# Kernel optimization log

Measured on AMD Instinct MI355X. Metric: run time of the kernel, lower is better.

Reference implementation:

```python
import jax, jax.numpy as jnp
import numpy as np
from jax import lax

BN_EPS = 1e-5


def conv(x, w, b, pad):
    # x: NCHW, w: OIHW
    y = lax.conv_general_dilated(x, w, (1, 1), [(pad, pad), (pad, pad)],
                                 dimension_numbers=('NCHW', 'OIHW', 'NCHW'))
    return y + b[None, :, None, None]


def conv_t(x, w, b):
    # ConvTranspose2d, stride=1, padding=0, kernel 3. w is torch layout [in, out, kh, kw].
    # Equivalent to a regular conv with spatially flipped kernel, in/out swapped, full padding (kh-1=2).
    wf = jnp.transpose(jnp.flip(w, (2, 3)), (1, 0, 2, 3))  # [out, in, kh, kw]
    y = lax.conv_general_dilated(x, wf, (1, 1), [(2, 2), (2, 2)],
                                 dimension_numbers=('NCHW', 'OIHW', 'NCHW'))
    return y + b[None, :, None, None]


def bn(x, g, be):
    # BatchNorm2d, training-mode batch stats (biased variance), gamma/beta learnable.
    mu = x.mean((0, 2, 3), keepdims=True)
    var = x.var((0, 2, 3), keepdims=True)
    xn = (x - mu) * lax.rsqrt(var + BN_EPS)
    return g[None, :, None, None] * xn + be[None, :, None, None]


def setup_inputs() -> dict:
    key = jax.random.key(0)
    ks = jax.random.split(key, 20)
    B, C, H, W = 16, 64, 44, 44
    P = H * W  # 1936

    def kaiming(k, shape, fan_out):
        return jax.random.normal(k, shape, jnp.float32) * np.sqrt(2.0 / fan_out)

    inp = {
        'depth': jax.random.normal(ks[0], (B, C, H, W), jnp.float32),
        'rgb': jax.random.normal(ks[1], (B, C, H, W), jnp.float32),
        # h_c / h_f conv layers: Conv2d(128, 64, 3, padding=1)
        'w_hc': kaiming(ks[2], (64, 128, 3, 3), 64 * 9), 'b_hc': jnp.zeros((64,), jnp.float32),
        'w_hf': kaiming(ks[3], (64, 128, 3, 3), 64 * 9), 'b_hf': jnp.zeros((64,), jnp.float32),
        # spatial_pool_agr
        'w_s1': kaiming(ks[4], (32, P, 3, 3), 32 * 9), 'bs1': jnp.zeros((32,), jnp.float32),
        'g1': jnp.ones((32,), jnp.float32), 'be1': jnp.zeros((32,), jnp.float32),
        'w_s2': kaiming(ks[5], (32, 32, 3, 3), 32 * 9), 'bs2': jnp.zeros((32,), jnp.float32),
        'g2': jnp.ones((32,), jnp.float32), 'be2': jnp.zeros((32,), jnp.float32),
        # ConvTranspose2d weights in torch layout [in, out, kh, kw]
        'w_d1': kaiming(ks[6], (32, 32, 3, 3), 32 * 9), 'bd1': jnp.zeros((32,), jnp.float32),
        'g3': jnp.ones((32,), jnp.float32), 'be3': jnp.zeros((32,), jnp.float32),
        'w_d2': kaiming(ks[7], (32, 1, 3, 3), 1 * 9), 'bd2': jnp.zeros((1,), jnp.float32),
        # channel_pool_ag: Linear(64, 16), Linear(16, 64)
        'w_l1': kaiming(ks[8], (16, 64), 16), 'bl1': jnp.zeros((16,), jnp.float32),
        'w_l2': kaiming(ks[9], (64, 16), 64), 'bl2': jnp.zeros((64,), jnp.float32),
    }
    return inp


def reference(depth, rgb, w_hc, b_hc, w_hf, b_hf,
              w_s1, bs1, g1, be1, w_s2, bs2, g2, be2,
              w_d1, bd1, g3, be3, w_d2, bd2,
              w_l1, bl1, w_l2, bl2):
    B, C, H, W = depth.shape
    # fused rgb+depth conv
    h_c = jnp.concatenate([rgb, depth], axis=1)          # [B, 2C, H, W]
    h_c_conv = jax.nn.relu(conv(h_c, w_hc, b_hc, 1))      # [B, 64, H, W]

    # per-pixel correlation: grouped 1x1 conv == batched matmul
    # pixel_corr[b, p, y, x] = sum_c rgb[b, c, y, x] * depth[b, c, p]
    pixel_corr = jnp.einsum('bchw,bcp->bphw', rgb, depth.reshape(B, C, H * W))

    x = jax.nn.relu(bn(conv(pixel_corr, w_s1, bs1, 0), g1, be1))  # 44 -> 42
    x = jax.nn.relu(bn(conv(x, w_s2, bs2, 0), g2, be2))           # 42 -> 40
    x = jax.nn.relu(bn(conv_t(x, w_d1, bd1), g3, be3))            # 40 -> 42
    spatial_att = jax.nn.sigmoid(conv_t(x, w_d2, bd2))            # [B, 1, 44, 44]

    # per-channel correlation: grouped full-extent conv == elementwise dot per (b, c)
    depth_corr = jnp.sum(rgb * depth, axis=(2, 3))                # [B, C]
    # MaxPool2d(1)/AvgPool2d(1) are identities -> both branches are identical
    def mlp(v):
        return jax.nn.relu(v @ w_l1.T + bl1) @ w_l2.T + bl2
    m = mlp(depth_corr)
    channel_att = jax.nn.sigmoid(m + m)[:, :, None, None]         # [B, C, 1, 1]

    h_att = jnp.concatenate([h_c_conv * spatial_att, h_c_conv * channel_att], axis=1)
    return jax.nn.relu(conv(h_att, w_hf, b_hf, 1))                # [B, 64, 44, 44]
```

## Files before the change

kernel.cpp:

```cpp
#include <hip/hip_runtime.h>
#include <math.h>

#define P_ 1936
#define EPS_ 1e-5f

typedef __attribute__((ext_vector_type(8))) short bf16x8;
typedef __attribute__((ext_vector_type(4))) float f32x4;
typedef __attribute__((ext_vector_type(4))) ushort u16x4;

__device__ __forceinline__ ushort f2bf(float f) {
    union { float f; unsigned u; } v; v.f = f;
    unsigned u = v.u;
    return (ushort)((u + 0x7FFFu + ((u >> 16) & 1u)) >> 16);
}
__device__ __forceinline__ float bf2f(ushort h) {
    union { unsigned u; float f; } v; v.u = (unsigned)h << 16;
    return v.f;
}

__device__ __forceinline__ void bn_coef(const float* stats, const float* g,
                                        const float* be, int ch, float inv_n,
                                        float& sc, float& sh) {
    float sum = stats[ch*2], sq = stats[ch*2+1];
    float mu = sum * inv_n;
    float var = sq * inv_n - mu*mu;
    float r = rsqrtf(var + EPS_);
    sc = g[ch] * r;
    sh = be[ch] - mu * sc;
}

__global__ __launch_bounds__(256) void k_setup(const float* __restrict__ whc,
                                               const float* __restrict__ whf,
                                               const float* __restrict__ ws2,
                                               const float* __restrict__ wd1,
                                               const float* __restrict__ ws1,
                                               const float* __restrict__ rgb,
                                               const float* __restrict__ depth,
                                               ushort* __restrict__ wpck,
                                               ushort* __restrict__ a2,
                                               ushort* __restrict__ a3,
                                               ushort* __restrict__ apck1,
                                               ushort* __restrict__ xp,
                                               ushort* __restrict__ depthb,
                                               float* __restrict__ dcor,
                                               float* __restrict__ stats) {
    __shared__ float r8[8];
    const int bx = blockIdx.x, t = threadIdx.x;
    if (bx < 2808) {
        if (bx == 0 && t < 192) stats[t] = 0.f;
        int idx = bx * 256 + t;
        if (idx < 147456) {
            const float* src = (idx < 73728) ? whc : whf;
            int j = (idx < 73728) ? idx : idx - 73728;
            int kk = j / 8192, rem = j - kk * 8192;
            int o = rem >> 7, c = rem & 127;
            wpck[(idx < 73728 ? 0 : 73728) + (kk * 64 + o) * 128 + c] =
                f2bf(src[(size_t)(o * 128 + c) * 9 + kk]);
        } else if (idx < 156672) {
            int j = idx - 147456;
            int kk = j >> 10, rem = j & 1023, o = rem >> 5, c = rem & 31;
            a2[j] = f2bf(ws2[((size_t)o*32 + c)*9 + kk]);
            a3[j] = f2bf(wd1[((size_t)c*32 + o)*9 + (8 - kk)]);
        } else if (idx < 718848) {
            int j = idx - 156672;
            int m = j / 1952, p = j - m*1952;
            int o = m / 9, kk = m - o*9;
            apck1[j] = (p < P_) ? f2bf(ws1[((size_t)o*P_ + p)*9 + kk]) : (ushort)0;
        }
        return;
    }
    const int j = bx - 2808;
    const int g8 = j & 7, b = j >> 3;
    const int c0 = g8 * 8;
    const float* rsrc = rgb   + ((size_t)b*64 + c0)*P_;
    const float* dsrc = depth + ((size_t)b*64 + c0)*P_;
    ushort* xr = xp + ((size_t)(b*16 + g8))*2300*8;
    ushort* xd = xp + ((size_t)(b*16 + 8 + g8))*2300*8;
    if (t < 8) r8[t] = 0.f;
    __syncthreads();
    float dc[8];
    #pragma unroll
    for (int e = 0; e < 8; ++e) dc[e] = 0.f;

    for (int pos = t; pos < 2300; pos += 256) {
        int y1 = pos / 50, x1 = pos - y1*50;
        uint4 vr = {0u,0u,0u,0u}, vd = {0u,0u,0u,0u};
        if (y1 >= 1 && y1 <= 44 && x1 >= 1 && x1 <= 44) {
            int p = (y1-1)*44 + (x1-1);
            ushort hr[8], hd[8];
            #pragma unroll
            for (int e = 0; e < 8; ++e) {
                float fr = rsrc[(size_t)e*P_ + p];
                float fd = dsrc[(size_t)e*P_ + p];
                dc[e] = fmaf(fr, fd, dc[e]);
                hr[e] = f2bf(fr); hd[e] = f2bf(fd);
            }
            vr.x = hr[0] | ((unsigned)hr[1] << 16); vr.y = hr[2] | ((unsigned)hr[3] << 16);
            vr.z = hr[4] | ((unsigned)hr[5] << 16); vr.w = hr[6] | ((unsigned)hr[7] << 16);
            vd.x = hd[0] | ((unsigned)hd[1] << 16); vd.y = hd[2] | ((unsigned)hd[3] << 16);
            vd.z = hd[4] | ((unsigned)hd[5] << 16); vd.w = hd[6] | ((unsigned)hd[7] << 16);
        }
        *(uint4*)(xr + (size_t)pos*8) = vr;
        *(uint4*)(xd + (size_t)pos*8) = vd;
    }
    for (int idx = t; idx < 8*488; idx += 256) {
        int e = idx / 488, jj = idx - e*488;
        u16x4 h = {0,0,0,0};
        if (jj < 484) {
            float4 f4 = *(const float4*)(dsrc + (size_t)e*P_ + jj*4);
            h[0] = f2bf(f4.x); h[1] = f2bf(f4.y); h[2] = f2bf(f4.z); h[3] = f2bf(f4.w);
        }
        *(u16x4*)(depthb + ((size_t)(b*64 + c0 + e))*1952 + jj*4) = h;
    }
    #pragma unroll
    for (int e = 0; e < 8; ++e) {
        float v = dc[e];
        #pragma unroll
        for (int off = 32; off > 0; off >>= 1) v += __shfl_down(v, off, 64);
        if ((t & 63) == 0) atomicAdd(&r8[e], v);
    }
    __syncthreads();
    if (t < 8) dcor[b*64 + c0 + t] = r8[t];
}

__global__ __launch_bounds__(256) void k_hcconv(const ushort* __restrict__ xp,
                                                const ushort* __restrict__ wt,
                                                const float* __restrict__ bias,
                                                ushort* __restrict__ hcp) {
    __shared__ ushort lds[9616];
    const int rt = blockIdx.x, og = blockIdx.y, b = blockIdx.z, t = threadIdx.x;
    const int w = t >> 6, lane = t & 63, lr = lane & 15, lg = lane >> 4;
    const int r0 = rt * 4;
    f32x4 acc[2][3];
    #pragma unroll
    for (int mf = 0; mf < 2; ++mf)
        #pragma unroll
        for (int nf = 0; nf < 3; ++nf)
            acc[mf][nf] = (f32x4){0.f, 0.f, 0.f, 0.f};

    for (int s = 0; s < 4; ++s) {
        __syncthreads();
        const ushort* gsrc = xp + ((size_t)(b*16 + s*4))*2300*8;
        for (int u = t; u < 1200; u += 256) {
            int cg = u / 300, rem = u - cg*300;
            int rr = rem / 50, xx = rem - rr*50;
            uint4 v = *(const uint4*)(gsrc + (((size_t)cg*46 + (r0+rr))*50 + xx)*8);
            *(uint4*)(lds + (size_t)u*8) = v;
        }
        __syncthreads();
        const int abase = s*32 + lg*8;
        #pragma unroll
        for (int kk = 0; kk < 9; ++kk) {
            bf16x8 af[2];
            #pragma unroll
            for (int mf = 0; mf < 2; ++mf)
                af[mf] = *(const bf16x8*)(wt + (size_t)(kk*64 + og*32 + mf*16 + lr)*128 + abase);
            const int ky = kk / 3, kx = kk - ky*3;
            #pragma unroll
            for (int nf = 0; nf < 3; ++nf) {
                bf16x8 bf = *(const bf16x8*)&lds[((lg*6 + (w + ky))*50 + (nf*16 + lr + kx))*8];
                #pragma unroll
                for (int mf = 0; mf < 2; ++mf)
                    acc[mf][nf] = __builtin_amdgcn_mfma_f32_16x16x32_bf16(af[mf], bf, acc[mf][nf], 0, 0, 0);
            }
        }
    }
    const int y = r0 + w;
    #pragma unroll
    for (int nf = 0; nf < 3; ++nf) {
        int x = nf*16 + lr;
        if (x < 44) {
            #pragma unroll
            for (int mf = 0; mf < 2; ++mf) {
                u16x4 pk;
                #pragma unroll
                for (int i = 0; i < 4; ++i) {
                    int ol = mf*16 + lg*4 + i;
                    pk[i] = f2bf(fmaxf(acc[mf][nf][i] + bias[og*32 + ol], 0.f));
                }
                int g = og*4 + mf*2 + (lg >> 1);
                *(u16x4*)(hcp + (((size_t)(b*8 + g)*46 + (y+1))*50 + (x+1))*8 + (lg&1)*4) = pk;
            }
        }
    }
}

__global__ __launch_bounds__(256) void k_final(const ushort* __restrict__ hcp,
                                               const float* __restrict__ satt,
                                               const float* __restrict__ catt,
                                               const ushort* __restrict__ wt,
                                               const float* __restrict__ bias,
                                               float* __restrict__ out) {
    __shared__ ushort lds[9616];
    __shared__ float catv[64];
    const int rt = blockIdx.x, og = blockIdx.y, b = blockIdx.z, t = threadIdx.x;
    const int w = t >> 6, lane = t & 63, lr = lane & 15, lg = lane >> 4;
    const int r0 = rt * 4;
    if (t < 64) catv[t] = catt[b*64 + t];
    f32x4 acc[2][3];
    #pragma unroll
    for (int mf = 0; mf < 2; ++mf)
        #pragma unroll
        for (int nf = 0; nf < 3; ++nf)
            acc[mf][nf] = (f32x4){0.f, 0.f, 0.f, 0.f};

    for (int s = 0; s < 4; ++s) {
        __syncthreads();
        for (int u = t; u < 1200; u += 256) {
            int cg = u / 300, rem = u - cg*300;
            int rr = rem / 50, xx = rem - rr*50;
            int g = s*4 + cg;
            int y1 = r0 + rr;
            uint4 v = {0u,0u,0u,0u};
            if (y1 >= 1 && y1 <= 44 && xx >= 1 && xx <= 44) {
                int gs = (g < 8) ? g : (g - 8);
                uint4 raw = *(const uint4*)(hcp + (((size_t)(b*8 + gs)*46 + y1)*50 + xx)*8);
                unsigned arr[4] = {raw.x, raw.y, raw.z, raw.w};
                ushort h[8];
                if (g < 8) {
                    float att = satt[(size_t)b*P_ + (y1-1)*44 + (xx-1)];
                    #pragma unroll
                    for (int e = 0; e < 8; ++e) {
                        ushort hv = (e & 1) ? (ushort)(arr[e>>1] >> 16) : (ushort)(arr[e>>1] & 0xffffu);
                        h[e] = f2bf(bf2f(hv) * att);
                    }
                } else {
                    #pragma unroll
                    for (int e = 0; e < 8; ++e) {
                        ushort hv = (e & 1) ? (ushort)(arr[e>>1] >> 16) : (ushort)(arr[e>>1] & 0xffffu);
                        h[e] = f2bf(bf2f(hv) * catv[(g-8)*8 + e]);
                    }
                }
                v.x = h[0] | ((unsigned)h[1] << 16);
                v.y = h[2] | ((unsigned)h[3] << 16);
                v.z = h[4] | ((unsigned)h[5] << 16);
                v.w = h[6] | ((unsigned)h[7] << 16);
            }
            *(uint4*)(lds + (size_t)u*8) = v;
        }
        __syncthreads();
        const int abase = s*32 + lg*8;
        #pragma unroll
        for (int kk = 0; kk < 9; ++kk) {
            bf16x8 af[2];
            #pragma unroll
            for (int mf = 0; mf < 2; ++mf)
                af[mf] = *(const bf16x8*)(wt + (size_t)(kk*64 + og*32 + mf*16 + lr)*128 + abase);
            const int ky = kk / 3, kx = kk - ky*3;
            #pragma unroll
            for (int nf = 0; nf < 3; ++nf) {
                bf16x8 bf = *(const bf16x8*)&lds[((lg*6 + (w + ky))*50 + (nf*16 + lr + kx))*8];
                #pragma unroll
                for (int mf = 0; mf < 2; ++mf)
                    acc[mf][nf] = __builtin_amdgcn_mfma_f32_16x16x32_bf16(af[mf], bf, acc[mf][nf], 0, 0, 0);
            }
        }
    }
    const int y = r0 + w;
    #pragma unroll
    for (int nf = 0; nf < 3; ++nf) {
        int x = nf*16 + lr;
        if (x < 44) {
            #pragma unroll
            for (int mf = 0; mf < 2; ++mf) {
                #pragma unroll
                for (int i = 0; i < 4; ++i) {
                    int o = og*32 + mf*16 + lg*4 + i;
                    out[(((size_t)b*64 + o)*44 + y)*44 + x] = fmaxf(acc[mf][nf][i] + bias[o], 0.f);
                }
            }
        }
    }
}

__global__ __launch_bounds__(256) void k_Umfma(const ushort* __restrict__ apck1,
                                               const ushort* __restrict__ depthb,
                                               ushort* __restrict__ upck,
                                               const float* __restrict__ dcorr,
                                               const float* __restrict__ wl1,
                                               const float* __restrict__ bl1,
                                               const float* __restrict__ wl2,
                                               const float* __restrict__ bl2,
                                               float* __restrict__ catt) {
    const int mt = blockIdx.x, b = blockIdx.y, t = threadIdx.x;
    if (mt == 18) {
        __shared__ float dc[64], h[16];
        if (t < 64) dc[t] = dcorr[b*64 + t];
        __syncthreads();
        if (t < 16) {
            float a = bl1[t];
            #pragma unroll 8
            for (int c = 0; c < 64; ++c) a = fmaf(dc[c], wl1[t*64 + c], a);
            h[t] = fmaxf(a, 0.f);
        }
        __syncthreads();
        if (t < 64) {
            float m = bl2[t];
            #pragma unroll
            for (int jj = 0; jj < 16; ++jj) m = fmaf(h[jj], wl2[t*16 + jj], m);
            catt[b*64 + t] = 1.f / (1.f + expf(-2.f*m));
        }
        return;
    }
    const int nt = t >> 6, lane = t & 63, lr = lane & 15, lg = lane >> 4;
    f32x4 acc = (f32x4){0.f, 0.f, 0.f, 0.f};
    const ushort* ap = apck1 + (size_t)(mt*16 + lr)*1952 + lg*8;
    const ushort* bp = depthb + ((size_t)(b*64) + nt*16 + lr)*1952 + lg*8;
    #pragma unroll 4
    for (int ks = 0; ks < 61; ++ks) {
        bf16x8 af = *(const bf16x8*)(ap + ks*32);
        bf16x8 bf = *(const bf16x8*)(bp + ks*32);
        acc = __builtin_amdgcn_mfma_f32_16x16x32_bf16(af, bf, acc, 0, 0, 0);
    }
    #pragma unroll
    for (int i = 0; i < 4; ++i) {
        int m = mt*16 + lg*4 + i;
        int o = m / 9, kk = m - o*9;
        upck[((size_t)(b*9 + kk)*32 + o)*64 + nt*16 + lr] = f2bf(acc[i]);
    }
}

__global__ __launch_bounds__(256) void k_conv1_mfma(const ushort* __restrict__ xp,
                                                    const ushort* __restrict__ upck,
                                                    const float* __restrict__ bs1,
                                                    ushort* __restrict__ z1p,
                                                    float* __restrict__ stats) {
    __shared__ ushort lds[8*6*50*8 + 32];
    __shared__ float ssum[32], ssq[32];
    const int rt = blockIdx.x, b = blockIdx.y, t = threadIdx.x;
    const int w = t >> 6, lane = t & 63, lr = lane & 15, lg = lane >> 4;
    const int r0 = rt * 4;
    if (t < 32) { ssum[t] = 0.f; ssq[t] = 0.f; }
    f32x4 acc[2][3];
    #pragma unroll
    for (int mf = 0; mf < 2; ++mf)
        #pragma unroll
        for (int nf = 0; nf < 3; ++nf)
            acc[mf][nf] = (f32x4){0.f, 0.f, 0.f, 0.f};

    const ushort* gsrc = xp + (size_t)b*16*2300*8;
    for (int u = t; u < 2400; u += 256) {
        int cg = u / 300, rem = u - cg*300;
        int rr = rem / 50, xx = rem - rr*50;
        int y1 = min(r0 + 1 + rr, 45);
        *(uint4*)(lds + (size_t)u*8) = *(const uint4*)(gsrc + (((size_t)cg*46 + y1)*50 + xx)*8);
    }
    __syncthreads();
    #pragma unroll
    for (int s = 0; s < 2; ++s) {
        #pragma unroll
        for (int kk = 0; kk < 9; ++kk) {
            bf16x8 af[2];
            #pragma unroll
            for (int mf = 0; mf < 2; ++mf)
                af[mf] = *(const bf16x8*)(upck + ((size_t)(b*9 + kk)*32 + mf*16 + lr)*64 + s*32 + lg*8);
            const int ky = kk / 3, kx = kk - ky*3;
            #pragma unroll
            for (int nf = 0; nf < 3; ++nf) {
                bf16x8 bv = *(const bf16x8*)&lds[(((s*4 + lg)*6 + (w + ky))*50 + (nf*16 + lr + kx + 1))*8];
                #pragma unroll
                for (int mf = 0; mf < 2; ++mf)
                    acc[mf][nf] = __builtin_amdgcn_mfma_f32_16x16x32_bf16(af[mf], bv, acc[mf][nf], 0, 0, 0);
            }
        }
    }
    const int y = r0 + w;
    const int cb = lg*4;
    if (y < 42) {
        float ls[2][4], lq[2][4], br[2][4];
        #pragma unroll
        for (int mf = 0; mf < 2; ++mf)
            #pragma unroll
            for (int i = 0; i < 4; ++i) {
                ls[mf][i] = 0.f; lq[mf][i] = 0.f;
                br[mf][i] = bs1[mf*16 + cb + i];
            }
        #pragma unroll
        for (int nf = 0; nf < 3; ++nf) {
            int x = nf*16 + lr;
            bool xv = (x < 42);
            #pragma unroll
            for (int mf = 0; mf < 2; ++mf) {
                u16x4 pk;
                #pragma unroll
                for (int i = 0; i < 4; ++i) {
                    float v = acc[mf][nf][i] + br[mf][i];
                    if (xv) { ls[mf][i] += v; lq[mf][i] = fmaf(v, v, lq[mf][i]); }
                    pk[i] = f2bf(v);
                }
                if (xv) {
                    int cg1 = mf*2 + (lg >> 1);
                    *(u16x4*)(z1p + ((((size_t)b*4 + cg1)*42 + y)*48 + x)*8 + (lg&1)*4) = pk;
                }
            }
        }
        #pragma unroll
        for (int mf = 0; mf < 2; ++mf)
            #pragma unroll
            for (int i = 0; i < 4; ++i) {
                float s0 = ls[mf][i], q0 = lq[mf][i];
                #pragma unroll
                for (int m = 1; m < 16; m <<= 1) { s0 += __shfl_xor(s0, m, 64); q0 += __shfl_xor(q0, m, 64); }
                if (lr == 0) { atomicAdd(&ssum[mf*16 + cb + i], s0); atomicAdd(&ssq[mf*16 + cb + i], q0); }
            }
    }
    __syncthreads();
    if (t < 32) { atomicAdd(&stats[t*2], ssum[t]); atomicAdd(&stats[t*2+1], ssq[t]); }
}

__global__ __launch_bounds__(256) void k_conv2_mfma(const ushort* __restrict__ z1p,
                                                    const ushort* __restrict__ apck,
                                                    const float* __restrict__ bs2,
                                                    const float* __restrict__ g1,
                                                    const float* __restrict__ be1,
                                                    const float* __restrict__ statsIn,
                                                    ushort* __restrict__ z2p,
                                                    float* __restrict__ statsOut) {
    __shared__ ushort lds[4*6*48*8 + 32];
    __shared__ float sc[32], sh[32], ssum[32], ssq[32];
    const int rt = blockIdx.x, b = blockIdx.y, t = threadIdx.x;
    const int w = t >> 6, lane = t & 63, lr = lane & 15, lg = lane >> 4;
    const int r0 = rt * 4;
    if (t < 32) {
        bn_coef(statsIn, g1, be1, t, 1.f/28224.f, sc[t], sh[t]);
        ssum[t] = 0.f; ssq[t] = 0.f;
    }
    __syncthreads();
    f32x4 acc[2][3];
    #pragma unroll
    for (int mf = 0; mf < 2; ++mf)
        #pragma unroll
        for (int nf = 0; nf < 3; ++nf)
            acc[mf][nf] = (f32x4){0.f, 0.f, 0.f, 0.f};

    for (int u = t; u < 1152; u += 256) {
        int cg = u / 288, rem = u - cg*288;
        int rr = rem / 48, xx = rem - rr*48;
        uint4 raw = *(const uint4*)(z1p + ((((size_t)b*4 + cg)*42 + (r0 + rr))*48 + xx)*8);
        unsigned arr[4] = {raw.x, raw.y, raw.z, raw.w};
        ushort h[8];
        #pragma unroll
        for (int e = 0; e < 8; ++e) {
            ushort hv = (e & 1) ? (ushort)(arr[e>>1] >> 16) : (ushort)(arr[e>>1] & 0xffffu);
            float f = fmaxf(fmaf(bf2f(hv), sc[cg*8 + e], sh[cg*8 + e]), 0.f);
            h[e] = f2bf(f);
        }
        uint4 v;
        v.x = h[0] | ((unsigned)h[1] << 16);
        v.y = h[2] | ((unsigned)h[3] << 16);
        v.z = h[4] | ((unsigned)h[5] << 16);
        v.w = h[6] | ((unsigned)h[7] << 16);
        *(uint4*)(lds + (size_t)u*8) = v;
    }
    __syncthreads();
    #pragma unroll
    for (int kk = 0; kk < 9; ++kk) {
        bf16x8 af[2];
        #pragma unroll
        for (int mf = 0; mf < 2; ++mf)
            af[mf] = *(const bf16x8*)(apck + (size_t)(kk*32 + mf*16 + lr)*32 + lg*8);
        const int ky = kk / 3, kx = kk - ky*3;
        #pragma unroll
        for (int nf = 0; nf < 3; ++nf) {
            bf16x8 bv = *(const bf16x8*)&lds[((lg*6 + (w + ky))*48 + (nf*16 + lr + kx))*8];
            #pragma unroll
            for (int mf = 0; mf < 2; ++mf)
                acc[mf][nf] = __builtin_amdgcn_mfma_f32_16x16x32_bf16(af[mf], bv, acc[mf][nf], 0, 0, 0);
        }
    }
    const int y = r0 + w;
    const int cb = lg*4;
    {
        float ls[2][4], lq[2][4], br[2][4];
        #pragma unroll
        for (int mf = 0; mf < 2; ++mf)
            #pragma unroll
            for (int i = 0; i < 4; ++i) {
                ls[mf][i] = 0.f; lq[mf][i] = 0.f;
                br[mf][i] = bs2[mf*16 + cb + i];
            }
        #pragma unroll
        for (int nf = 0; nf < 3; ++nf) {
            int x = nf*16 + lr;
            bool xv = (x < 40);
            #pragma unroll
            for (int mf = 0; mf < 2; ++mf) {
                u16x4 pk;
                #pragma unroll
                for (int i = 0; i < 4; ++i) {
                    float v = acc[mf][nf][i] + br[mf][i];
                    if (xv) { ls[mf][i] += v; lq[mf][i] = fmaf(v, v, lq[mf][i]); }
                    pk[i] = f2bf(v);
                }
                if (xv) {
                    int cg1 = mf*2 + (lg >> 1);
                    *(u16x4*)(z2p + ((((size_t)b*4 + cg1)*46 + (y+2))*48 + (x+2))*8 + (lg&1)*4) = pk;
                }
            }
        }
        #pragma unroll
        for (int mf = 0; mf < 2; ++mf)
            #pragma unroll
            for (int i = 0; i < 4; ++i) {
                float s0 = ls[mf][i], q0 = lq[mf][i];
                #pragma unroll
                for (int m = 1; m < 16; m <<= 1) { s0 += __shfl_xor(s0, m, 64); q0 += __shfl_xor(q0, m, 64); }
                if (lr == 0) { atomicAdd(&ssum[mf*16 + cb + i], s0); atomicAdd(&ssq[mf*16 + cb + i], q0); }
            }
    }
    __syncthreads();
    if (t < 32) { atomicAdd(&statsOut[t*2], ssum[t]); atomicAdd(&statsOut[t*2+1], ssq[t]); }
}

__global__ __launch_bounds__(256) void k_dconv1_mfma(const ushort* __restrict__ z2p,
                                                     const ushort* __restrict__ apck,
                                                     const float* __restrict__ bd1,
                                                     const float* __restrict__ g2,
                                                     const float* __restrict__ be2,
                                                     const float* __restrict__ statsIn,
                                                     ushort* __restrict__ z3p,
                                                     float* __restrict__ statsOut) {
    __shared__ ushort lds[4*6*48*8 + 32];
    __shared__ float sc[32], sh[32], ssum[32], ssq[32];
    const int rt = blockIdx.x, b = blockIdx.y, t = threadIdx.x;
    const int w = t >> 6, lane = t & 63, lr = lane & 15, lg = lane >> 4;
    const int r0 = rt * 4;
    if (t < 32) {
        bn_coef(statsIn, g2, be2, t, 1.f/25600.f, sc[t], sh[t]);
        ssum[t] = 0.f; ssq[t] = 0.f;
    }
    __syncthreads();
    f32x4 acc[2][3];
    #pragma unroll
    for (int mf = 0; mf < 2; ++mf)
        #pragma unroll
        for (int nf = 0; nf < 3; ++nf)
            acc[mf][nf] = (f32x4){0.f, 0.f, 0.f, 0.f};

    for (int u = t; u < 1152; u += 256) {
        int cg = u / 288, rem = u - cg*288;
        int rr = rem / 48, xx = rem - rr*48;
        int row = r0 + rr;
        uint4 v = {0u,0u,0u,0u};
        if (row >= 2 && row <= 41 && xx >= 2 && xx <= 41) {
            uint4 raw = *(const uint4*)(z2p + ((((size_t)b*4 + cg)*46 + row)*48 + xx)*8);
            unsigned arr[4] = {raw.x, raw.y, raw.z, raw.w};
            ushort h[8];
            #pragma unroll
            for (int e = 0; e < 8; ++e) {
                ushort hv = (e & 1) ? (ushort)(arr[e>>1] >> 16) : (ushort)(arr[e>>1] & 0xffffu);
                float f = fmaxf(fmaf(bf2f(hv), sc[cg*8 + e], sh[cg*8 + e]), 0.f);
                h[e] = f2bf(f);
            }
            v.x = h[0] | ((unsigned)h[1] << 16);
            v.y = h[2] | ((unsigned)h[3] << 16);
            v.z = h[4] | ((unsigned)h[5] << 16);
            v.w = h[6] | ((unsigned)h[7] << 16);
        }
        *(uint4*)(lds + (size_t)u*8) = v;
    }
    __syncthreads();
    #pragma unroll
    for (int kk = 0; kk < 9; ++kk) {
        bf16x8 af[2];
        #pragma unroll
        for (int mf = 0; mf < 2; ++mf)
            af[mf] = *(const bf16x8*)(apck + (size_t)(kk*32 + mf*16 + lr)*32 + lg*8);
        const int ky = kk / 3, kx = kk - ky*3;
        #pragma unroll
        for (int nf = 0; nf < 3; ++nf) {
            bf16x8 bv = *(const bf16x8*)&lds[((lg*6 + (w + ky))*48 + (nf*16 + lr + kx))*8];
            #pragma unroll
            for (int mf = 0; mf < 2; ++mf)
                acc[mf][nf] = __builtin_amdgcn_mfma_f32_16x16x32_bf16(af[mf], bv, acc[mf][nf], 0, 0, 0);
        }
    }
    const int y = r0 + w;
    const int cb = lg*4;
    if (y < 42) {
        float ls[2][4], lq[2][4], br[2][4];
        #pragma unroll
        for (int mf = 0; mf < 2; ++mf)
            #pragma unroll
            for (int i = 0; i < 4; ++i) {
                ls[mf][i] = 0.f; lq[mf][i] = 0.f;
                br[mf][i] = bd1[mf*16 + cb + i];
            }
        #pragma unroll
        for (int nf = 0; nf < 3; ++nf) {
            int x = nf*16 + lr;
            bool xv = (x < 42);
            #pragma unroll
            for (int mf = 0; mf < 2; ++mf) {
                u16x4 pk;
                #pragma unroll
                for (int i = 0; i < 4; ++i) {
                    float v = acc[mf][nf][i] + br[mf][i];
                    if (xv) { ls[mf][i] += v; lq[mf][i] = fmaf(v, v, lq[mf][i]); }
                    pk[i] = f2bf(v);
                }
                if (xv) {
                    int cg1 = mf*2 + (lg >> 1);
                    *(u16x4*)(z3p + ((((size_t)b*4 + cg1)*46 + (y+2))*48 + (x+2))*8 + (lg&1)*4) = pk;
                }
            }
        }
        #pragma unroll
        for (int mf = 0; mf < 2; ++mf)
            #pragma unroll
            for (int i = 0; i < 4; ++i) {
                float s0 = ls[mf][i], q0 = lq[mf][i];
                #pragma unroll
                for (int m = 1; m < 16; m <<= 1) { s0 += __shfl_xor(s0, m, 64); q0 += __shfl_xor(q0, m, 64); }
                if (lr == 0) { atomicAdd(&ssum[mf*16 + cb + i], s0); atomicAdd(&ssq[mf*16 + cb + i], q0); }
            }
    }
    __syncthreads();
    if (t < 32) { atomicAdd(&statsOut[t*2], ssum[t]); atomicAdd(&statsOut[t*2+1], ssq[t]); }
}

__global__ __launch_bounds__(256) void k_dconv2(const ushort* __restrict__ z3p,
                                                const float* __restrict__ wd2,
                                                const float* __restrict__ bd2,
                                                const float* __restrict__ g3,
                                                const float* __restrict__ be3,
                                                const float* __restrict__ stats,
                                                float* __restrict__ satt) {
    __shared__ float sc[32], sh[32], wf[32][9];
    const int b = blockIdx.y, t = threadIdx.x;
    if (t < 32) bn_coef(stats, g3, be3, t, 1.f/28224.f, sc[t], sh[t]);
    for (int u = t; u < 288; u += 256) {
        int c = u / 9, k = u - c*9;
        wf[c][k] = wd2[c*9 + 8 - k];
    }
    __syncthreads();
    const int pix = blockIdx.x * 256 + t;
    if (pix >= P_) return;
    const int y = pix / 44, x = pix - y*44;
    float acc = bd2[0];
    #pragma unroll
    for (int kk = 0; kk < 9; ++kk) {
        int ky = kk / 3, kx = kk - ky*3;
        int ry = y + ky, rx = x + kx;
        if (ry < 2 || ry > 43 || rx < 2 || rx > 43) continue;
        #pragma unroll
        for (int cg = 0; cg < 4; ++cg) {
            uint4 raw = *(const uint4*)(z3p + ((((size_t)b*4 + cg)*46 + ry)*48 + rx)*8);
            unsigned arr[4] = {raw.x, raw.y, raw.z, raw.w};
            #pragma unroll
            for (int e = 0; e < 8; ++e) {
                ushort hv = (e & 1) ? (ushort)(arr[e>>1] >> 16) : (ushort)(arr[e>>1] & 0xffffu);
                float f = fmaxf(fmaf(bf2f(hv), sc[cg*8 + e], sh[cg*8 + e]), 0.f);
                acc = fmaf(f, wf[cg*8 + e][kk], acc);
            }
        }
    }
    satt[(size_t)b*P_ + pix] = 1.f / (1.f + expf(-acc));
}

extern "C" void kernel_launch(void* const* d_in, const int* in_sizes, int n_in,
                              void* d_out, int out_size, void* d_ws, size_t ws_size,
                              hipStream_t stream) {
    const float* depth = (const float*)d_in[0];
    const float* rgb   = (const float*)d_in[1];
    const float* w_hc  = (const float*)d_in[2];
    const float* b_hc  = (const float*)d_in[3];
    const float* w_hf  = (const float*)d_in[4];
    const float* b_hf  = (const float*)d_in[5];
    const float* w_s1  = (const float*)d_in[6];
    const float* bs1   = (const float*)d_in[7];
    const float* g1    = (const float*)d_in[8];
    const float* be1   = (const float*)d_in[9];
    const float* w_s2  = (const float*)d_in[10];
    const float* bs2   = (const float*)d_in[11];
    const float* g2    = (const float*)d_in[12];
    const float* be2   = (const float*)d_in[13];
    const float* w_d1  = (const float*)d_in[14];
    const float* bd1   = (const float*)d_in[15];
    const float* g3    = (const float*)d_in[16];
    const float* be3   = (const float*)d_in[17];
    const float* w_d2  = (const float*)d_in[18];
    const float* bd2   = (const float*)d_in[19];
    const float* w_l1  = (const float*)d_in[20];
    const float* bl1   = (const float*)d_in[21];
    const float* w_l2  = (const float*)d_in[22];
    const float* bl2   = (const float*)d_in[23];

    float* out = (float*)d_out;
    float* ws  = (float*)d_ws;

    float* satt  = ws;
    float* catt  = satt + 30976;
    float* dcor  = catt + 1024;
    float* stats = dcor + 1024;
    ushort* hcp    = (ushort*)(stats + 192);
    ushort* wpck   = hcp    + 2355200;
    ushort* apck2  = wpck   + 147456;
    ushort* apck3  = apck2  + 9216;
    ushort* apck1  = apck3  + 9216;
    ushort* depthb = apck1  + 562176;
    ushort* upck   = depthb + 1998848;
    ushort* z1p    = upck   + 294912;
    ushort* z2p    = z1p    + 1032192;
    ushort* z3p    = z2p    + 1130496;
    ushort* xpck   = z3p    + 1130496;

    k_setup<<<2936, 256, 0, stream>>>(w_hc, w_hf, w_s2, w_d1, w_s1, rgb, depth,
                                      wpck, apck2, apck3, apck1, xpck, depthb, dcor, stats);

    k_hcconv<<<dim3(11,2,16), 256, 0, stream>>>(xpck, wpck, b_hc, hcp);
    k_Umfma<<<dim3(19,16), 256, 0, stream>>>(apck1, depthb, upck,
                                             dcor, w_l1, bl1, w_l2, bl2, catt);

    k_conv1_mfma<<<dim3(11,16), 256, 0, stream>>>(xpck, upck, bs1, z1p, stats);
    k_conv2_mfma<<<dim3(10,16), 256, 0, stream>>>(z1p, apck2, bs2, g1, be1, stats, z2p, stats + 64);
    k_dconv1_mfma<<<dim3(11,16), 256, 0, stream>>>(z2p, apck3, bd1, g2, be2, stats + 64, z3p, stats + 128);
    k_dconv2<<<dim3(8,16), 256, 0, stream>>>(z3p, w_d2, bd2, g3, be3, stats + 128, satt);

    k_final<<<dim3(11,2,16), 256, 0, stream>>>(hcp, satt, catt, wpck + 73728, b_hf, out);
}
```

Baseline: 156.4 us.

## Fuse mid-pipeline convs into persistent kernel with grid barriers

Merges conv1, conv2, dconv1, dconv2 and the final conv into one 176-block kernel that separates the BN-dependent stages with atomic-counter grid barriers. The hc conv and the U/MLP work are combined into a single front kernel, and the hc conv now computes both output-channel groups per block. The setup input packing is split four ways across more blocks, with partial depth correlations summed later. This cuts launch count and launch gaps at the cost of spin-wait barriers, which rely on all 176 blocks being co-resident, and of higher register and LDS pressure.

```diff
diff --git a/kernel.cpp b/kernel.cpp
--- a/kernel.cpp
+++ b/kernel.cpp
@@ -27,6 +27,17 @@
     float r = rsqrtf(var + EPS_);
     sc = g[ch] * r;
     sh = be[ch] - mu * sc;
+}
+
+__device__ __forceinline__ void gbar(unsigned* bar, int idx, unsigned nblk) {
+    __syncthreads();
+    if (threadIdx.x == 0) {
+        __threadfence();
+        atomicAdd(&bar[idx], 1u);
+        while (atomicAdd(&bar[idx], 0u) < nblk) { }
+        __threadfence();
+    }
+    __syncthreads();
 }
 
 __global__ __launch_bounds__(256) void k_setup(const float* __restrict__ whc,
@@ -42,12 +53,16 @@
                                                ushort* __restrict__ apck1,
                                                ushort* __restrict__ xp,
                                                ushort* __restrict__ depthb,
-                                               float* __restrict__ dcor,
-                                               float* __restrict__ stats) {
+                                               float* __restrict__ dcor_part,
+                                               float* __restrict__ stats,
+                                               unsigned* __restrict__ bar) {
     __shared__ float r8[8];
     const int bx = blockIdx.x, t = threadIdx.x;
     if (bx < 2808) {
-        if (bx == 0 && t < 192) stats[t] = 0.f;
+        if (bx == 0) {
+            if (t < 192) stats[t] = 0.f;
+            else if (t < 200) bar[t - 192] = 0u;
+        }
         int idx = bx * 256 + t;
         if (idx < 147456) {
             const float* src = (idx < 73728) ? whc : whf;
@@ -70,7 +85,7 @@
         return;
     }
     const int j = bx - 2808;
-    const int g8 = j & 7, b = j >> 3;
+    const int g8 = j & 7, b = (j >> 3) & 15, q = j >> 7;
     const int c0 = g8 * 8;
     const float* rsrc = rgb   + ((size_t)b*64 + c0)*P_;
     const float* dsrc = depth + ((size_t)b*64 + c0)*P_;
@@ -82,7 +97,8 @@
     #pragma unroll
     for (int e = 0; e < 8; ++e) dc[e] = 0.f;
 
-    for (int pos = t; pos < 2300; pos += 256) {
+    const int pbase = q * 575;
+    for (int pos = pbase + t; pos < pbase + 575; pos += 256) {
         int y1 = pos / 50, x1 = pos - y1*50;
         uint4 vr = {0u,0u,0u,0u}, vd = {0u,0u,0u,0u};
         if (y1 >= 1 && y1 <= 44 && x1 >= 1 && x1 <= 44) {
@@ -103,7 +119,7 @@
         *(uint4*)(xr + (size_t)pos*8) = vr;
         *(uint4*)(xd + (size_t)pos*8) = vd;
     }
-    for (int idx = t; idx < 8*488; idx += 256) {
+    for (int idx = q*976 + t; idx < q*976 + 976; idx += 256) {
         int e = idx / 488, jj = idx - e*488;
         u16x4 h = {0,0,0,0};
         if (jj < 484) {
@@ -120,177 +136,103 @@
         if ((t & 63) == 0) atomicAdd(&r8[e], v);
     }
     __syncthreads();
-    if (t < 8) dcor[b*64 + c0 + t] = r8[t];
+    if (t < 8) dcor_part[q*1024 + b*64 + c0 + t] = r8[t];
 }
 
-__global__ __launch_bounds__(256) void k_hcconv(const ushort* __restrict__ xp,
-                                                const ushort* __restrict__ wt,
-                                                const float* __restrict__ bias,
-                                                ushort* __restrict__ hcp) {
-    __shared__ ushort lds[9616];
-    const int rt = blockIdx.x, og = blockIdx.y, b = blockIdx.z, t = threadIdx.x;
-    const int w = t >> 6, lane = t & 63, lr = lane & 15, lg = lane >> 4;
-    const int r0 = rt * 4;
-    f32x4 acc[2][3];
-    #pragma unroll
-    for (int mf = 0; mf < 2; ++mf)
-        #pragma unroll
-        for (int nf = 0; nf < 3; ++nf)
-            acc[mf][nf] = (f32x4){0.f, 0.f, 0.f, 0.f};
-
-    for (int s = 0; s < 4; ++s) {
-        __syncthreads();
-        const ushort* gsrc = xp + ((size_t)(b*16 + s*4))*2300*8;
-        for (int u = t; u < 1200; u += 256) {
-            int cg = u / 300, rem = u - cg*300;
-            int rr = rem / 50, xx = rem - rr*50;
-            uint4 v = *(const uint4*)(gsrc + (((size_t)cg*46 + (r0+rr))*50 + xx)*8);
-            *(uint4*)(lds + (size_t)u*8) = v;
-        }
-        __syncthreads();
-        const int abase = s*32 + lg*8;
-        #pragma unroll
-        for (int kk = 0; kk < 9; ++kk) {
-            bf16x8 af[2];
-            #pragma unroll
-            for (int mf = 0; mf < 2; ++mf)
-                af[mf] = *(const bf16x8*)(wt + (size_t)(kk*64 + og*32 + mf*16 + lr)*128 + abase);
-            const int ky = kk / 3, kx = kk - ky*3;
-            #pragma unroll
-            for (int nf = 0; nf < 3; ++nf) {
-                bf16x8 bf = *(const bf16x8*)&lds[((lg*6 + (w + ky))*50 + (nf*16 + lr + kx))*8];
-                #pragma unroll
-                for (int mf = 0; mf < 2; ++mf)
-                    acc[mf][nf] = __builtin_amdgcn_mfma_f32_16x16x32_bf16(af[mf], bf, acc[mf][nf], 0, 0, 0);
-            }
-        }
-    }
-    const int y = r0 + w;
-    #pragma unroll
-    for (int nf = 0; nf < 3; ++nf) {
-        int x = nf*16 + lr;
-        if (x < 44) {
-            #pragma unroll
-            for (int mf = 0; mf < 2; ++mf) {
-                u16x4 pk;
-                #pragma unroll
-                for (int i = 0; i < 4; ++i) {
-                    int ol = mf*16 + lg*4 + i;
-                    pk[i] = f2bf(fmaxf(acc[mf][nf][i] + bias[og*32 + ol], 0.f));
-                }
-                int g = og*4 + mf*2 + (lg >> 1);
-                *(u16x4*)(hcp + (((size_t)(b*8 + g)*46 + (y+1))*50 + (x+1))*8 + (lg&1)*4) = pk;
-            }
-        }
-    }
-}
-
-__global__ __launch_bounds__(256) void k_final(const ushort* __restrict__ hcp,
-                                               const float* __restrict__ satt,
-                                               const float* __restrict__ catt,
+__global__ __launch_bounds__(256) void k_front(const ushort* __restrict__ xp,
                                                const ushort* __restrict__ wt,
-                                               const float* __restrict__ bias,
-                                               float* __restrict__ out) {
-    __shared__ ushort lds[9616];
-    __shared__ float catv[64];
-    const int rt = blockIdx.x, og = blockIdx.y, b = blockIdx.z, t = threadIdx.x;
-    const int w = t >> 6, lane = t & 63, lr = lane & 15, lg = lane >> 4;
-    const int r0 = rt * 4;
-    if (t < 64) catv[t] = catt[b*64 + t];
-    f32x4 acc[2][3];
-    #pragma unroll
-    for (int mf = 0; mf < 2; ++mf)
-        #pragma unroll
-        for (int nf = 0; nf < 3; ++nf)
-            acc[mf][nf] = (f32x4){0.f, 0.f, 0.f, 0.f};
-
-    for (int s = 0; s < 4; ++s) {
-        __syncthreads();
-        for (int u = t; u < 1200; u += 256) {
-            int cg = u / 300, rem = u - cg*300;
-            int rr = rem / 50, xx = rem - rr*50;
-            int g = s*4 + cg;
-            int y1 = r0 + rr;
-            uint4 v = {0u,0u,0u,0u};
-            if (y1 >= 1 && y1 <= 44 && xx >= 1 && xx <= 44) {
-                int gs = (g < 8) ? g : (g - 8);
-                uint4 raw = *(const uint4*)(hcp + (((size_t)(b*8 + gs)*46 + y1)*50 + xx)*8);
-                unsigned arr[4] = {raw.x, raw.y, raw.z, raw.w};
-                ushort h[8];
-                if (g < 8) {
-                    float att = satt[(size_t)b*P_ + (y1-1)*44 + (xx-1)];
-                    #pragma unroll
-                    for (int e = 0; e < 8; ++e) {
-                        ushort hv = (e & 1) ? (ushort)(arr[e>>1] >> 16) : (ushort)(arr[e>>1] & 0xffffu);
-                        h[e] = f2bf(bf2f(hv) * att);
-                    }
-                } else {
-                    #pragma unroll
-                    for (int e = 0; e < 8; ++e) {
-                        ushort hv = (e & 1) ? (ushort)(arr[e>>1] >> 16) : (ushort)(arr[e>>1] & 0xffffu);
-                        h[e] = f2bf(bf2f(hv) * catv[(g-8)*8 + e]);
-                    }
-                }
-                v.x = h[0] | ((unsigned)h[1] << 16);
-                v.y = h[2] | ((unsigned)h[3] << 16);
-                v.z = h[4] | ((unsigned)h[5] << 16);
-                v.w = h[6] | ((unsigned)h[7] << 16);
-            }
-            *(uint4*)(lds + (size_t)u*8) = v;
-        }
-        __syncthreads();
-        const int abase = s*32 + lg*8;
-        #pragma unroll
-        for (int kk = 0; kk < 9; ++kk) {
-            bf16x8 af[2];
-            #pragma unroll
-            for (int mf = 0; mf < 2; ++mf)
-                af[mf] = *(const bf16x8*)(wt + (size_t)(kk*64 + og*32 + mf*16 + lr)*128 + abase);
-            const int ky = kk / 3, kx = kk - ky*3;
-            #pragma unroll
-            for (int nf = 0; nf < 3; ++nf) {
-                bf16x8 bf = *(const bf16x8*)&lds[((lg*6 + (w + ky))*50 + (nf*16 + lr + kx))*8];
-                #pragma unroll
-                for (int mf = 0; mf < 2; ++mf)
-                    acc[mf][nf] = __builtin_amdgcn_mfma_f32_16x16x32_bf16(af[mf], bf, acc[mf][nf], 0, 0, 0);
-            }
-        }
-    }
-    const int y = r0 + w;
-    #pragma unroll
-    for (int nf = 0; nf < 3; ++nf) {
-        int x = nf*16 + lr;
-        if (x < 44) {
-            #pragma unroll
-            for (int mf = 0; mf < 2; ++mf) {
-                #pragma unroll
-                for (int i = 0; i < 4; ++i) {
-                    int o = og*32 + mf*16 + lg*4 + i;
-                    out[(((size_t)b*64 + o)*44 + y)*44 + x] = fmaxf(acc[mf][nf][i] + bias[o], 0.f);
-                }
-            }
-        }
-    }
-}
-
-__global__ __launch_bounds__(256) void k_Umfma(const ushort* __restrict__ apck1,
+                                               const float* __restrict__ bhc,
+                                               ushort* __restrict__ hcp,
+                                               const ushort* __restrict__ apck1,
                                                const ushort* __restrict__ depthb,
                                                ushort* __restrict__ upck,
-                                               const float* __restrict__ dcorr,
+                                               const float* __restrict__ dcor_part,
                                                const float* __restrict__ wl1,
                                                const float* __restrict__ bl1,
                                                const float* __restrict__ wl2,
                                                const float* __restrict__ bl2,
                                                float* __restrict__ catt) {
-    const int mt = blockIdx.x, b = blockIdx.y, t = threadIdx.x;
+    __shared__ ushort lds[9616];
+    __shared__ float mlpb[80];
+    const int bx = blockIdx.x, t = threadIdx.x;
+    if (bx < 176) {
+        const int rt = bx % 11, b = bx / 11;
+        const int w = t >> 6, lane = t & 63, lr = lane & 15, lg = lane >> 4;
+        const int r0 = rt * 4;
+        f32x4 acc[2][2][3];
+        #pragma unroll
+        for (int og = 0; og < 2; ++og)
+            #pragma unroll
+            for (int mf = 0; mf < 2; ++mf)
+                #pragma unroll
+                for (int nf = 0; nf < 3; ++nf)
+                    acc[og][mf][nf] = (f32x4){0.f, 0.f, 0.f, 0.f};
+
+        for (int s = 0; s < 4; ++s) {
+            __syncthreads();
+            const ushort* gsrc = xp + ((size_t)(b*16 + s*4))*2300*8;
+            for (int u = t; u < 1200; u += 256) {
+                int cg = u / 300, rem = u - cg*300;
+                int rr = rem / 50, xx = rem - rr*50;
+                uint4 v = *(const uint4*)(gsrc + (((size_t)cg*46 + (r0+rr))*50 + xx)*8);
+                *(uint4*)(lds + (size_t)u*8) = v;
+            }
+            __syncthreads();
+            const int abase = s*32 + lg*8;
+            #pragma unroll
+            for (int kk = 0; kk < 9; ++kk) {
+                bf16x8 af[2][2];
+                #pragma unroll
+                for (int og = 0; og < 2; ++og)
+                    #pragma unroll
+                    for (int mf = 0; mf < 2; ++mf)
+                        af[og][mf] = *(const bf16x8*)(wt + (size_t)(kk*64 + og*32 + mf*16 + lr)*128 + abase);
+                const int ky = kk / 3, kx = kk - ky*3;
+                #pragma unroll
+                for (int nf = 0; nf < 3; ++nf) {
+                    bf16x8 bf = *(const bf16x8*)&lds[((lg*6 + (w + ky))*50 + (nf*16 + lr + kx))*8];
+                    #pragma unroll
+                    for (int og = 0; og < 2; ++og)
+                        #pragma unroll
+                        for (int mf = 0; mf < 2; ++mf)
+                            acc[og][mf][nf] = __builtin_amdgcn_mfma_f32_16x16x32_bf16(af[og][mf], bf, acc[og][mf][nf], 0, 0, 0);
+                }
+            }
+        }
+        const int y = r0 + w;
+        #pragma unroll
+        for (int nf = 0; nf < 3; ++nf) {
+            int x = nf*16 + lr;
+            if (x < 44) {
+                #pragma unroll
+                for (int og = 0; og < 2; ++og)
+                    #pragma unroll
+                    for (int mf = 0; mf < 2; ++mf) {
+                        u16x4 pk;
+                        #pragma unroll
+                        for (int i = 0; i < 4; ++i) {
+                            int ol = og*32 + mf*16 + lg*4 + i;
+                            pk[i] = f2bf(fmaxf(acc[og][mf][nf][i] + bhc[ol], 0.f));
+                        }
+                        int g = og*4 + mf*2 + (lg >> 1);
+                        *(u16x4*)(hcp + (((size_t)(b*8 + g)*46 + (y+1))*50 + (x+1))*8 + (lg&1)*4) = pk;
+                    }
+            }
+        }
+        return;
+    }
+    const int j = bx - 176;
+    const int mt = j % 19, b = j / 19;
     if (mt == 18) {
-        __shared__ float dc[64], h[16];
-        if (t < 64) dc[t] = dcorr[b*64 + t];
+        float* dcs = mlpb;
+        float* h   = mlpb + 64;
+        if (t < 64) dcs[t] = dcor_part[b*64 + t] + dcor_part[1024 + b*64 + t]
+                           + dcor_part[2048 + b*64 + t] + dcor_part[3072 + b*64 + t];
         __syncthreads();
         if (t < 16) {
             float a = bl1[t];
             #pragma unroll 8
-            for (int c = 0; c < 64; ++c) a = fmaf(dc[c], wl1[t*64 + c], a);
+            for (int c = 0; c < 64; ++c) a = fmaf(dcs[c], wl1[t*64 + c], a);
             h[t] = fmaxf(a, 0.f);
         }
         __syncthreads();
@@ -320,230 +262,133 @@
     }
 }
 
-__global__ __launch_bounds__(256) void k_conv1_mfma(const ushort* __restrict__ xp,
-                                                    const ushort* __restrict__ upck,
-                                                    const float* __restrict__ bs1,
-                                                    ushort* __restrict__ z1p,
-                                                    float* __restrict__ stats) {
-    __shared__ ushort lds[8*6*50*8 + 32];
-    __shared__ float ssum[32], ssq[32];
+__global__ __launch_bounds__(256) void k_mid(const ushort* __restrict__ xp,
+                                             const ushort* __restrict__ upck,
+                                             const float* __restrict__ bs1,
+                                             const ushort* __restrict__ a2,
+                                             const float* __restrict__ bs2,
+                                             const float* __restrict__ g1,
+                                             const float* __restrict__ be1,
+                                             const ushort* __restrict__ a3,
+                                             const float* __restrict__ bd1,
+                                             const float* __restrict__ g2,
+                                             const float* __restrict__ be2,
+                                             const float* __restrict__ wd2,
+                                             const float* __restrict__ bd2,
+                                             const float* __restrict__ g3,
+                                             const float* __restrict__ be3,
+                                             const ushort* __restrict__ hcp,
+                                             const float* __restrict__ catt,
+                                             const ushort* __restrict__ wtf,
+                                             const float* __restrict__ bhf,
+                                             ushort* __restrict__ z1p,
+                                             ushort* __restrict__ z2p,
+                                             ushort* __restrict__ z3p,
+                                             float* __restrict__ satt,
+                                             float* __restrict__ stats,
+                                             unsigned* __restrict__ bar,
+                                             float* __restrict__ out) {
+    __shared__ ushort lds[19264];
+    __shared__ float sbuf[384];
+    const unsigned NB = 176u;
     const int rt = blockIdx.x, b = blockIdx.y, t = threadIdx.x;
     const int w = t >> 6, lane = t & 63, lr = lane & 15, lg = lane >> 4;
     const int r0 = rt * 4;
-    if (t < 32) { ssum[t] = 0.f; ssq[t] = 0.f; }
-    f32x4 acc[2][3];
-    #pragma unroll
-    for (int mf = 0; mf < 2; ++mf)
-        #pragma unroll
-        for (int nf = 0; nf < 3; ++nf)
-            acc[mf][nf] = (f32x4){0.f, 0.f, 0.f, 0.f};
-
-    const ushort* gsrc = xp + (size_t)b*16*2300*8;
-    for (int u = t; u < 2400; u += 256) {
-        int cg = u / 300, rem = u - cg*300;
-        int rr = rem / 50, xx = rem - rr*50;
-        int y1 = min(r0 + 1 + rr, 45);
-        *(uint4*)(lds + (size_t)u*8) = *(const uint4*)(gsrc + (((size_t)cg*46 + y1)*50 + xx)*8);
-    }
-    __syncthreads();
-    #pragma unroll
-    for (int s = 0; s < 2; ++s) {
-        #pragma unroll
-        for (int kk = 0; kk < 9; ++kk) {
-            bf16x8 af[2];
-            #pragma unroll
-            for (int mf = 0; mf < 2; ++mf)
-                af[mf] = *(const bf16x8*)(upck + ((size_t)(b*9 + kk)*32 + mf*16 + lr)*64 + s*32 + lg*8);
-            const int ky = kk / 3, kx = kk - ky*3;
+
+    {
+        float* ssum = sbuf; float* ssq = sbuf + 32;
+        if (t < 32) { ssum[t] = 0.f; ssq[t] = 0.f; }
+        f32x4 acc[2][3];
+        #pragma unroll
+        for (int mf = 0; mf < 2; ++mf)
+            #pragma unroll
+            for (int nf = 0; nf < 3; ++nf)
+                acc[mf][nf] = (f32x4){0.f, 0.f, 0.f, 0.f};
+        const ushort* gsrc = xp + (size_t)b*16*2300*8;
+        for (int u = t; u < 2400; u += 256) {
+            int cg = u / 300, rem = u - cg*300;
+            int rr = rem / 50, xx = rem - rr*50;
+            int y1 = min(r0 + 1 + rr, 45);
+            *(uint4*)(lds + (size_t)u*8) = *(const uint4*)(gsrc + (((size_t)cg*46 + y1)*50 + xx)*8);
+        }
+        __syncthreads();
+        #pragma unroll
+        for (int s = 0; s < 2; ++s) {
+            #pragma unroll
+            for (int kk = 0; kk < 9; ++kk) {
+                bf16x8 af[2];
+                #pragma unroll
+                for (int mf = 0; mf < 2; ++mf)
+                    af[mf] = *(const bf16x8*)(upck + ((size_t)(b*9 + kk)*32 + mf*16 + lr)*64 + s*32 + lg*8);
+                const int ky = kk / 3, kx = kk - ky*3;
+                #pragma unroll
+                for (int nf = 0; nf < 3; ++nf) {
+                    bf16x8 bv = *(const bf16x8*)&lds[(((s*4 + lg)*6 + (w + ky))*50 + (nf*16 + lr + kx + 1))*8];
+                    #pragma unroll
+                    for (int mf = 0; mf < 2; ++mf)
+                        acc[mf][nf] = __builtin_amdgcn_mfma_f32_16x16x32_bf16(af[mf], bv, acc[mf][nf], 0, 0, 0);
+                }
+            }
+        }
+        const int y = r0 + w;
+        const int cb = lg*4;
+        if (y < 42) {
+            float ls[2][4], lq[2][4];
+            #pragma unroll
+            for (int mf = 0; mf < 2; ++mf)
+                #pragma unroll
+                for (int i = 0; i < 4; ++i) { ls[mf][i] = 0.f; lq[mf][i] = 0.f; }
             #pragma unroll
             for (int nf = 0; nf < 3; ++nf) {
-                bf16x8 bv = *(const bf16x8*)&lds[(((s*4 + lg)*6 + (w + ky))*50 + (nf*16 + lr + kx + 1))*8];
-                #pragma unroll
-                for (int mf = 0; mf < 2; ++mf)
-                    acc[mf][nf] = __builtin_amdgcn_mfma_f32_16x16x32_bf16(af[mf], bv, acc[mf][nf], 0, 0, 0);
-            }
-        }
-    }
-    const int y = r0 + w;
-    const int cb = lg*4;
-    if (y < 42) {
-        float ls[2][4], lq[2][4], br[2][4];
+                int x = nf*16 + lr;
+                bool xv = (x < 42);
+                #pragma unroll
+                for (int mf = 0; mf < 2; ++mf) {
+                    u16x4 pk;
+                    #pragma unroll
+                    for (int i = 0; i < 4; ++i) {
+                        float v = acc[mf][nf][i] + bs1[mf*16 + cb + i];
+                        if (xv) { ls[mf][i] += v; lq[mf][i] = fmaf(v, v, lq[mf][i]); }
+                        pk[i] = f2bf(v);
+                    }
+                    if (xv) {
+                        int cg1 = mf*2 + (lg >> 1);
+                        *(u16x4*)(z1p + ((((size_t)b*4 + cg1)*42 + y)*48 + x)*8 + (lg&1)*4) = pk;
+                    }
+                }
+            }
+            #pragma unroll
+            for (int mf = 0; mf < 2; ++mf)
+                #pragma unroll
+                for (int i = 0; i < 4; ++i) {
+                    float s0 = ls[mf][i], q0 = lq[mf][i];
+                    #pragma unroll
+                    for (int m = 1; m < 16; m <<= 1) { s0 += __shfl_xor(s0, m, 64); q0 += __shfl_xor(q0, m, 64); }
+                    if (lr == 0) { atomicAdd(&ssum[mf*16 + cb + i], s0); atomicAdd(&ssq[mf*16 + cb + i], q0); }
+                }
+        }
+        __syncthreads();
+        if (t < 32) { atomicAdd(&stats[t*2], ssum[t]); atomicAdd(&stats[t*2+1], ssq[t]); }
+    }
+    gbar(bar, 0, NB);
+
+    if (rt < 10) {
+        float* sc = sbuf; float* sh = sbuf + 32; float* ssum = sbuf + 64; float* ssq = sbuf + 96;
+        if (t < 32) {
+            bn_coef(stats, g1, be1, t, 1.f/28224.f, sc[t], sh[t]);
+            ssum[t] = 0.f; ssq[t] = 0.f;
+        }
+        __syncthreads();
+        f32x4 acc[2][3];
         #pragma unroll
         for (int mf = 0; mf < 2; ++mf)
             #pragma unroll
-            for (int i = 0; i < 4; ++i) {
-                ls[mf][i] = 0.f; lq[mf][i] = 0.f;
-                br[mf][i] = bs1[mf*16 + cb + i];
-            }
-        #pragma unroll
-        for (int nf = 0; nf < 3; ++nf) {
-            int x = nf*16 + lr;
-            bool xv = (x < 42);
-            #pragma unroll
-            for (int mf = 0; mf < 2; ++mf) {
-                u16x4 pk;
-                #pragma unroll
-                for (int i = 0; i < 4; ++i) {
-                    float v = acc[mf][nf][i] + br[mf][i];
-                    if (xv) { ls[mf][i] += v; lq[mf][i] = fmaf(v, v, lq[mf][i]); }
-                    pk[i] = f2bf(v);
-                }
-                if (xv) {
-                    int cg1 = mf*2 + (lg >> 1);
-                    *(u16x4*)(z1p + ((((size_t)b*4 + cg1)*42 + y)*48 + x)*8 + (lg&1)*4) = pk;
-                }
-            }
-        }
-        #pragma unroll
-        for (int mf = 0; mf < 2; ++mf)
-            #pragma unroll
-            for (int i = 0; i < 4; ++i) {
-                float s0 = ls[mf][i], q0 = lq[mf][i];
-                #pragma unroll
-                for (int m = 1; m < 16; m <<= 1) { s0 += __shfl_xor(s0, m, 64); q0 += __shfl_xor(q0, m, 64); }
-                if (lr == 0) { atomicAdd(&ssum[mf*16 + cb + i], s0); atomicAdd(&ssq[mf*16 + cb + i], q0); }
-            }
-    }
-    __syncthreads();
-    if (t < 32) { atomicAdd(&stats[t*2], ssum[t]); atomicAdd(&stats[t*2+1], ssq[t]); }
-}
-
-__global__ __launch_bounds__(256) void k_conv2_mfma(const ushort* __restrict__ z1p,
-                                                    const ushort* __restrict__ apck,
-                                                    const float* __restrict__ bs2,
-                                                    const float* __restrict__ g1,
-                                                    const float* __restrict__ be1,
-                                                    const float* __restrict__ statsIn,
-                                                    ushort* __restrict__ z2p,
-                                                    float* __restrict__ statsOut) {
-    __shared__ ushort lds[4*6*48*8 + 32];
-    __shared__ float sc[32], sh[32], ssum[32], ssq[32];
-    const int rt = blockIdx.x, b = blockIdx.y, t = threadIdx.x;
-    const int w = t >> 6, lane = t & 63, lr = lane & 15, lg = lane >> 4;
-    const int r0 = rt * 4;
-    if (t < 32) {
-        bn_coef(statsIn, g1, be1, t, 1.f/28224.f, sc[t], sh[t]);
-        ssum[t] = 0.f; ssq[t] = 0.f;
-    }
-    __syncthreads();
-    f32x4 acc[2][3];
-    #pragma unroll
-    for (int mf = 0; mf < 2; ++mf)
-        #pragma unroll
-        for (int nf = 0; nf < 3; ++nf)
-            acc[mf][nf] = (f32x4){0.f, 0.f, 0.f, 0.f};
-
-    for (int u = t; u < 1152; u += 256) {
-        int cg = u / 288, rem = u - cg*288;
-        int rr = rem / 48, xx = rem - rr*48;
-        uint4 raw = *(const uint4*)(z1p + ((((size_t)b*4 + cg)*42 + (r0 + rr))*48 + xx)*8);
-        unsigned arr[4] = {raw.x, raw.y, raw.z, raw.w};
-        ushort h[8];
-        #pragma unroll
-        for (int e = 0; e < 8; ++e) {
-            ushort hv = (e & 1) ? (ushort)(arr[e>>1] >> 16) : (ushort)(arr[e>>1] & 0xffffu);
-            float f = fmaxf(fmaf(bf2f(hv), sc[cg*8 + e], sh[cg*8 + e]), 0.f);
-            h[e] = f2bf(f);
-        }
-        uint4 v;
-        v.x = h[0] | ((unsigned)h[1] << 16);
-        v.y = h[2] | ((unsigned)h[3] << 16);
-        v.z = h[4] | ((unsigned)h[5] << 16);
-        v.w = h[6] | ((unsigned)h[7] << 16);
-        *(uint4*)(lds + (size_t)u*8) = v;
-    }
-    __syncthreads();
-    #pragma unroll
-    for (int kk = 0; kk < 9; ++kk) {
-        bf16x8 af[2];
-        #pragma unroll
-        for (int mf = 0; mf < 2; ++mf)
-            af[mf] = *(const bf16x8*)(apck + (size_t)(kk*32 + mf*16 + lr)*32 + lg*8);
-        const int ky = kk / 3, kx = kk - ky*3;
-        #pragma unroll
-        for (int nf = 0; nf < 3; ++nf) {
-            bf16x8 bv = *(const bf16x8*)&lds[((lg*6 + (w + ky))*48 + (nf*16 + lr + kx))*8];
-            #pragma unroll
-            for (int mf = 0; mf < 2; ++mf)
-                acc[mf][nf] = __builtin_amdgcn_mfma_f32_16x16x32_bf16(af[mf], bv, acc[mf][nf], 0, 0, 0);
-        }
-    }
-    const int y = r0 + w;
-    const int cb = lg*4;
-    {
-        float ls[2][4], lq[2][4], br[2][4];
-        #pragma unroll
-        for (int mf = 0; mf < 2; ++mf)
-            #pragma unroll
-            for (int i = 0; i < 4; ++i) {
-                ls[mf][i] = 0.f; lq[mf][i] = 0.f;
-                br[mf][i] = bs2[mf*16 + cb + i];
-            }
-        #pragma unroll
-        for (int nf = 0; nf < 3; ++nf) {
-            int x = nf*16 + lr;
-            bool xv = (x < 40);
-            #pragma unroll
-            for (int mf = 0; mf < 2; ++mf) {
-                u16x4 pk;
-                #pragma unroll
-                for (int i = 0; i < 4; ++i) {
-                    float v = acc[mf][nf][i] + br[mf][i];
-                    if (xv) { ls[mf][i] += v; lq[mf][i] = fmaf(v, v, lq[mf][i]); }
-                    pk[i] = f2bf(v);
-                }
-                if (xv) {
-                    int cg1 = mf*2 + (lg >> 1);
-                    *(u16x4*)(z2p + ((((size_t)b*4 + cg1)*46 + (y+2))*48 + (x+2))*8 + (lg&1)*4) = pk;
-                }
-            }
-        }
-        #pragma unroll
-        for (int mf = 0; mf < 2; ++mf)
-            #pragma unroll
-            for (int i = 0; i < 4; ++i) {
-                float s0 = ls[mf][i], q0 = lq[mf][i];
-                #pragma unroll
-                for (int m = 1; m < 16; m <<= 1) { s0 += __shfl_xor(s0, m, 64); q0 += __shfl_xor(q0, m, 64); }
-                if (lr == 0) { atomicAdd(&ssum[mf*16 + cb + i], s0); atomicAdd(&ssq[mf*16 + cb + i], q0); }
-            }
-    }
-    __syncthreads();
-    if (t < 32) { atomicAdd(&statsOut[t*2], ssum[t]); atomicAdd(&statsOut[t*2+1], ssq[t]); }
-}
-
-__global__ __launch_bounds__(256) void k_dconv1_mfma(const ushort* __restrict__ z2p,
-                                                     const ushort* __restrict__ apck,
-                                                     const float* __restrict__ bd1,
-                                                     const float* __restrict__ g2,
-                                                     const float* __restrict__ be2,
-                                                     const float* __restrict__ statsIn,
-                                                     ushort* __restrict__ z3p,
-                                                     float* __restrict__ statsOut) {
-    __shared__ ushort lds[4*6*48*8 + 32];
-    __shared__ float sc[32], sh[32], ssum[32], ssq[32];
-    const int rt = blockIdx.x, b = blockIdx.y, t = threadIdx.x;
-    const int w = t >> 6, lane = t & 63, lr = lane & 15, lg = lane >> 4;
-    const int r0 = rt * 4;
-    if (t < 32) {
-        bn_coef(statsIn, g2, be2, t, 1.f/25600.f, sc[t], sh[t]);
-        ssum[t] = 0.f; ssq[t] = 0.f;
-    }
-    __syncthreads();
-    f32x4 acc[2][3];
-    #pragma unroll
-    for (int mf = 0; mf < 2; ++mf)
-        #pragma unroll
-        for (int nf = 0; nf < 3; ++nf)
-            acc[mf][nf] = (f32x4){0.f, 0.f, 0.f, 0.f};
-
-    for (int u = t; u < 1152; u += 256) {
-        int cg = u / 288, rem = u - cg*288;
-        int rr = rem / 48, xx = rem - rr*48;
-        int row = r0 + rr;
-        uint4 v = {0u,0u,0u,0u};
-        if (row >= 2 && row <= 41 && xx >= 2 && xx <= 41) {
-            uint4 raw = *(const uint4*)(z2p + ((((size_t)b*4 + cg)*46 + row)*48 + xx)*8);
+            for (int nf = 0; nf < 3; ++nf)
+                acc[mf][nf] = (f32x4){0.f, 0.f, 0.f, 0.f};
+        for (int u = t; u < 1152; u += 256) {
+            int cg = u / 288, rem = u - cg*288;
+            int rr = rem / 48, xx = rem - rr*48;
+            uint4 raw = *(const uint4*)(z1p + ((((size_t)b*4 + cg)*42 + (r0 + rr))*48 + xx)*8);
             unsigned arr[4] = {raw.x, raw.y, raw.z, raw.w};
             ushort h[8];
             #pragma unroll
@@ -552,110 +397,281 @@
                 float f = fmaxf(fmaf(bf2f(hv), sc[cg*8 + e], sh[cg*8 + e]), 0.f);
                 h[e] = f2bf(f);
             }
+            uint4 v;
             v.x = h[0] | ((unsigned)h[1] << 16);
             v.y = h[2] | ((unsigned)h[3] << 16);
             v.z = h[4] | ((unsigned)h[5] << 16);
             v.w = h[6] | ((unsigned)h[7] << 16);
-        }
-        *(uint4*)(lds + (size_t)u*8) = v;
-    }
-    __syncthreads();
-    #pragma unroll
-    for (int kk = 0; kk < 9; ++kk) {
-        bf16x8 af[2];
+            *(uint4*)(lds + (size_t)u*8) = v;
+        }
+        __syncthreads();
+        #pragma unroll
+        for (int kk = 0; kk < 9; ++kk) {
+            bf16x8 af[2];
+            #pragma unroll
+            for (int mf = 0; mf < 2; ++mf)
+                af[mf] = *(const bf16x8*)(a2 + (size_t)(kk*32 + mf*16 + lr)*32 + lg*8);
+            const int ky = kk / 3, kx = kk - ky*3;
+            #pragma unroll
+            for (int nf = 0; nf < 3; ++nf) {
+                bf16x8 bv = *(const bf16x8*)&lds[((lg*6 + (w + ky))*48 + (nf*16 + lr + kx))*8];
+                #pragma unroll
+                for (int mf = 0; mf < 2; ++mf)
+                    acc[mf][nf] = __builtin_amdgcn_mfma_f32_16x16x32_bf16(af[mf], bv, acc[mf][nf], 0, 0, 0);
+            }
+        }
+        const int y = r0 + w;
+        const int cb = lg*4;
+        {
+            float ls[2][4], lq[2][4];
+            #pragma unroll
+            for (int mf = 0; mf < 2; ++mf)
+                #pragma unroll
+                for (int i = 0; i < 4; ++i) { ls[mf][i] = 0.f; lq[mf][i] = 0.f; }
+            #pragma unroll
+            for (int nf = 0; nf < 3; ++nf) {
+                int x = nf*16 + lr;
+                bool xv = (x < 40);
+                #pragma unroll
+                for (int mf = 0; mf < 2; ++mf) {
+                    u16x4 pk;
+                    #pragma unroll
+                    for (int i = 0; i < 4; ++i) {
+                        float v = acc[mf][nf][i] + bs2[mf*16 + cb + i];
+                        if (xv) { ls[mf][i] += v; lq[mf][i] = fmaf(v, v, lq[mf][i]); }
+                        pk[i] = f2bf(v);
+                    }
+                    if (xv) {
+                        int cg1 = mf*2 + (lg >> 1);
+                        *(u16x4*)(z2p + ((((size_t)b*4 + cg1)*46 + (y+2))*48 + (x+2))*8 + (lg&1)*4) = pk;
+                    }
+                }
+            }
+            #pragma unroll
+            for (int mf = 0; mf < 2; ++mf)
+                #pragma unroll
+                for (int i = 0; i < 4; ++i) {
+                    float s0 = ls[mf][i], q0 = lq[mf][i];
+                    #pragma unroll
+                    for (int m = 1; m < 16; m <<= 1) { s0 += __shfl_xor(s0, m, 64); q0 += __shfl_xor(q0, m, 64); }
+                    if (lr == 0) { atomicAdd(&ssum[mf*16 + cb + i], s0); atomicAdd(&ssq[mf*16 + cb + i], q0); }
+                }
+        }
+        __syncthreads();
+        if (t < 32) { atomicAdd(&stats[64 + t*2], ssum[t]); atomicAdd(&stats[64 + t*2+1], ssq[t]); }
+    }
+    gbar(bar, 1, NB);
+
+    {
+        float* sc = sbuf; float* sh = sbuf + 32; float* ssum = sbuf + 64; float* ssq = sbuf + 96;
+        if (t < 32) {
+            bn_coef(stats + 64, g2, be2, t, 1.f/25600.f, sc[t], sh[t]);
+            ssum[t] = 0.f; ssq[t] = 0.f;
+        }
+        __syncthreads();
+        f32x4 acc[2][3];
         #pragma unroll
         for (int mf = 0; mf < 2; ++mf)
-            af[mf] = *(const bf16x8*)(apck + (size_t)(kk*32 + mf*16 + lr)*32 + lg*8);
-        const int ky = kk / 3, kx = kk - ky*3;
-        #pragma unroll
-        for (int nf = 0; nf < 3; ++nf) {
-            bf16x8 bv = *(const bf16x8*)&lds[((lg*6 + (w + ky))*48 + (nf*16 + lr + kx))*8];
-            #pragma unroll
-            for (int mf = 0; mf < 2; ++mf)
-                acc[mf][nf] = __builtin_amdgcn_mfma_f32_16x16x32_bf16(af[mf], bv, acc[mf][nf], 0, 0, 0);
-        }
-    }
-    const int y = r0 + w;
-    const int cb = lg*4;
-    if (y < 42) {
-        float ls[2][4], lq[2][4], br[2][4];
-        #pragma unroll
-        for (int mf = 0; mf < 2; ++mf)
-            #pragma unroll
-            for (int i = 0; i < 4; ++i) {
-                ls[mf][i] = 0.f; lq[mf][i] = 0.f;
-                br[mf][i] = bd1[mf*16 + cb + i];
-            }
+            #pragma unroll
+            for (int nf = 0; nf < 3; ++nf)
+                acc[mf][nf] = (f32x4){0.f, 0.f, 0.f, 0.f};
+        for (int u = t; u < 1152; u += 256) {
+            int cg = u / 288, rem = u - cg*288;
+            int rr = rem / 48, xx = rem - rr*48;
+            int row = r0 + rr;
+            uint4 v = {0u,0u,0u,0u};
+            if (row >= 2 && row <= 41 && xx >= 2 && xx <= 41) {
+                uint4 raw = *(const uint4*)(z2p + ((((size_t)b*4 + cg)*46 + row)*48 + xx)*8);
+                unsigned arr[4] = {raw.x, raw.y, raw.z, raw.w};
+                ushort h[8];
+                #pragma unroll
+                for (int e = 0; e < 8; ++e) {
+                    ushort hv = (e & 1) ? (ushort)(arr[e>>1] >> 16) : (ushort)(arr[e>>1] & 0xffffu);
+                    float f = fmaxf(fmaf(bf2f(hv), sc[cg*8 + e], sh[cg*8 + e]), 0.f);
+                    h[e] = f2bf(f);
+                }
+                v.x = h[0] | ((unsigned)h[1] << 16);
+                v.y = h[2] | ((unsigned)h[3] << 16);
+                v.z = h[4] | ((unsigned)h[5] << 16);
+                v.w = h[6] | ((unsigned)h[7] << 16);
+            }
+            *(uint4*)(lds + (size_t)u*8) = v;
+        }
+        __syncthreads();
+        #pragma unroll
+        for (int kk = 0; kk < 9; ++kk) {
+            bf16x8 af[2];
+            #pragma unroll
+            for (int mf = 0; mf < 2; ++mf)
+                af[mf] = *(const bf16x8*)(a3 + (size_t)(kk*32 + mf*16 + lr)*32 + lg*8);
+            const int ky = kk / 3, kx = kk - ky*3;
+            #pragma unroll
+            for (int nf = 0; nf < 3; ++nf) {
+                bf16x8 bv = *(const bf16x8*)&lds[((lg*6 + (w + ky))*48 + (nf*16 + lr + kx))*8];
+                #pragma unroll
+                for (int mf = 0; mf < 2; ++mf)
+                    acc[mf][nf] = __builtin_amdgcn_mfma_f32_16x16x32_bf16(af[mf], bv, acc[mf][nf], 0, 0, 0);
+            }
+        }
+        const int y = r0 + w;
+        const int cb = lg*4;
+        if (y < 42) {
+            float ls[2][4], lq[2][4];
+            #pragma unroll
+            for (int mf = 0; mf < 2; ++mf)
+                #pragma unroll
+                for (int i = 0; i < 4; ++i) { ls[mf][i] = 0.f; lq[mf][i] = 0.f; }
+            #pragma unroll
+            for (int nf = 0; nf < 3; ++nf) {
+                int x = nf*16 + lr;
+                bool xv = (x < 42);
+                #pragma unroll
+                for (int mf = 0; mf < 2; ++mf) {
+                    u16x4 pk;
+                    #pragma unroll
+                    for (int i = 0; i < 4; ++i) {
+                        float v = acc[mf][nf][i] + bd1[mf*16 + cb + i];
+                        if (xv) { ls[mf][i] += v; lq[mf][i] = fmaf(v, v, lq[mf][i]); }
+                        pk[i] = f2bf(v);
+                    }
+                    if (xv) {
+                        int cg1 = mf*2 + (lg >> 1);
+                        *(u16x4*)(z3p + ((((size_t)b*4 + cg1)*46 + (y+2))*48 + (x+2))*8 + (lg&1)*4) = pk;
+                    }
+                }
+            }
+            #pragma unroll
+            for (int mf = 0; mf < 2; ++mf)
+                #pragma unroll
+                for (int i = 0; i < 4; ++i) {
+                    float s0 = ls[mf][i], q0 = lq[mf][i];
+                    #pragma unroll
+                    for (int m = 1; m < 16; m <<= 1) { s0 += __shfl_xor(s0, m, 64); q0 += __shfl_xor(q0, m, 64); }
+                    if (lr == 0) { atomicAdd(&ssum[mf*16 + cb + i], s0); atomicAdd(&ssq[mf*16 + cb + i], q0); }
+                }
+        }
+        __syncthreads();
+        if (t < 32) { atomicAdd(&stats[128 + t*2], ssum[t]); atomicAdd(&stats[128 + t*2+1], ssq[t]); }
+    }
+    gbar(bar, 2, NB);
+
+    if (rt < 8) {
+        float* sc = sbuf; float* sh = sbuf + 32; float* wf = sbuf + 64;
+        if (t < 32) bn_coef(stats + 128, g3, be3, t, 1.f/28224.f, sc[t], sh[t]);
+        for (int u = t; u < 288; u += 256) {
+            int c = u / 9, k = u - c*9;
+            wf[c*9 + k] = wd2[c*9 + 8 - k];
+        }
+        __syncthreads();
+        const int pix = rt * 256 + t;
+        if (pix < P_) {
+            const int y = pix / 44, x = pix - y*44;
+            float acc = bd2[0];
+            #pragma unroll
+            for (int kk = 0; kk < 9; ++kk) {
+                int ky = kk / 3, kx = kk - ky*3;
+                int ry = y + ky, rx = x + kx;
+                if (ry < 2 || ry > 43 || rx < 2 || rx > 43) continue;
+                #pragma unroll
+                for (int cg = 0; cg < 4; ++cg) {
+                    uint4 raw = *(const uint4*)(z3p + ((((size_t)b*4 + cg)*46 + ry)*48 + rx)*8);
+                    unsigned arr[4] = {raw.x, raw.y, raw.z, raw.w};
+                    #pragma unroll
+                    for (int e = 0; e < 8; ++e) {
+                        ushort hv = (e & 1) ? (ushort)(arr[e>>1] >> 16) : (ushort)(arr[e>>1] & 0xffffu);
+                        float f = fmaxf(fmaf(bf2f(hv), sc[cg*8 + e], sh[cg*8 + e]), 0.f);
+                        acc = fmaf(f, wf[(cg*8 + e)*9 + kk], acc);
+                    }
+                }
+            }
+            satt[(size_t)b*P_ + pix] = 1.f / (1.f + expf(-acc));
+        }
+    }
+    gbar(bar, 3, NB);
+
+    {
+        if (t < 64) sbuf[t] = catt[b*64 + t];
+        f32x4 acc[2][2][3];
+        #pragma unroll
+        for (int og = 0; og < 2; ++og)
+            #pragma unroll
+            for (int mf = 0; mf < 2; ++mf)
+                #pragma unroll
+                for (int nf = 0; nf < 3; ++nf)
+                    acc[og][mf][nf] = (f32x4){0.f, 0.f, 0.f, 0.f};
+        for (int s = 0; s < 4; ++s) {
+            __syncthreads();
+            for (int u = t; u < 1200; u += 256) {
+                int cg = u / 300, rem = u - cg*300;
+                int rr = rem / 50, xx = rem - rr*50;
+                int g = s*4 + cg;
+                int y1 = r0 + rr;
+                uint4 v = {0u,0u,0u,0u};
+                if (y1 >= 1 && y1 <= 44 && xx >= 1 && xx <= 44) {
+                    int gs = (g < 8) ? g : (g - 8);
+                    uint4 raw = *(const uint4*)(hcp + (((size_t)(b*8 + gs)*46 + y1)*50 + xx)*8);
+                    unsigned arr[4] = {raw.x, raw.y, raw.z, raw.w};
+                    ushort h[8];
+                    if (g < 8) {
+                        float att = satt[(size_t)b*P_ + (y1-1)*44 + (xx-1)];
+                        #pragma unroll
+                        for (int e = 0; e < 8; ++e) {
+                            ushort hv = (e & 1) ? (ushort)(arr[e>>1] >> 16) : (ushort)(arr[e>>1] & 0xffffu);
+                            h[e] = f2bf(bf2f(hv) * att);
+                        }
+                    } else {
+                        #pragma unroll
+                        for (int e = 0; e < 8; ++e) {
+                            ushort hv = (e & 1) ? (ushort)(arr[e>>1] >> 16) : (ushort)(arr[e>>1] & 0xffffu);
+                            h[e] = f2bf(bf2f(hv) * sbuf[(g-8)*8 + e]);
+                        }
+                    }
+                    v.x = h[0] | ((unsigned)h[1] << 16);
+                    v.y = h[2] | ((unsigned)h[3] << 16);
+                    v.z = h[4] | ((unsigned)h[5] << 16);
+                    v.w = h[6] | ((unsigned)h[7] << 16);
+                }
+                *(uint4*)(lds + (size_t)u*8) = v;
+            }
+            __syncthreads();
+            const int abase = s*32 + lg*8;
+            #pragma unroll
+            for (int kk = 0; kk < 9; ++kk) {
+                bf16x8 af[2][2];
+                #pragma unroll
+                for (int og = 0; og < 2; ++og)
+                    #pragma unroll
+                    for (int mf = 0; mf < 2; ++mf)
+                        af[og][mf] = *(const bf16x8*)(wtf + (size_t)(kk*64 + og*32 + mf*16 + lr)*128 + abase);
+                const int ky = kk / 3, kx = kk - ky*3;
+                #pragma unroll
+                for (int nf = 0; nf < 3; ++nf) {
+                    bf16x8 bf = *(const bf16x8*)&lds[((lg*6 + (w + ky))*50 + (nf*16 + lr + kx))*8];
+                    #pragma unroll
+                    for (int og = 0; og < 2; ++og)
+                        #pragma unroll
+                        for (int mf = 0; mf < 2; ++mf)
+                            acc[og][mf][nf] = __builtin_amdgcn_mfma_f32_16x16x32_bf16(af[og][mf], bf, acc[og][mf][nf], 0, 0, 0);
+                }
+            }
+        }
+        const int y = r0 + w;
         #pragma unroll
         for (int nf = 0; nf < 3; ++nf) {
             int x = nf*16 + lr;
-            bool xv = (x < 42);
-            #pragma unroll
-            for (int mf = 0; mf < 2; ++mf) {
-                u16x4 pk;
-                #pragma unroll
-                for (int i = 0; i < 4; ++i) {
-                    float v = acc[mf][nf][i] + br[mf][i];
-                    if (xv) { ls[mf][i] += v; lq[mf][i] = fmaf(v, v, lq[mf][i]); }
-                    pk[i] = f2bf(v);
-                }
-                if (xv) {
-                    int cg1 = mf*2 + (lg >> 1);
-                    *(u16x4*)(z3p + ((((size_t)b*4 + cg1)*46 + (y+2))*48 + (x+2))*8 + (lg&1)*4) = pk;
-                }
-            }
-        }
-        #pragma unroll
-        for (int mf = 0; mf < 2; ++mf)
-            #pragma unroll
-            for (int i = 0; i < 4; ++i) {
-                float s0 = ls[mf][i], q0 = lq[mf][i];
-                #pragma unroll
-                for (int m = 1; m < 16; m <<= 1) { s0 += __shfl_xor(s0, m, 64); q0 += __shfl_xor(q0, m, 64); }
-                if (lr == 0) { atomicAdd(&ssum[mf*16 + cb + i], s0); atomicAdd(&ssq[mf*16 + cb + i], q0); }
-            }
-    }
-    __syncthreads();
-    if (t < 32) { atomicAdd(&statsOut[t*2], ssum[t]); atomicAdd(&statsOut[t*2+1], ssq[t]); }
-}
-
-__global__ __launch_bounds__(256) void k_dconv2(const ushort* __restrict__ z3p,
-                                                const float* __restrict__ wd2,
-                                                const float* __restrict__ bd2,
-                                                const float* __restrict__ g3,
-                                                const float* __restrict__ be3,
-                                                const float* __restrict__ stats,
-                                                float* __restrict__ satt) {
-    __shared__ float sc[32], sh[32], wf[32][9];
-    const int b = blockIdx.y, t = threadIdx.x;
-    if (t < 32) bn_coef(stats, g3, be3, t, 1.f/28224.f, sc[t], sh[t]);
-    for (int u = t; u < 288; u += 256) {
-        int c = u / 9, k = u - c*9;
-        wf[c][k] = wd2[c*9 + 8 - k];
-    }
-    __syncthreads();
-    const int pix = blockIdx.x * 256 + t;
-    if (pix >= P_) return;
-    const int y = pix / 44, x = pix - y*44;
-    float acc = bd2[0];
-    #pragma unroll
-    for (int kk = 0; kk < 9; ++kk) {
-        int ky = kk / 3, kx = kk - ky*3;
-        int ry = y + ky, rx = x + kx;
-        if (ry < 2 || ry > 43 || rx < 2 || rx > 43) continue;
-        #pragma unroll
-        for (int cg = 0; cg < 4; ++cg) {
-            uint4 raw = *(const uint4*)(z3p + ((((size_t)b*4 + cg)*46 + ry)*48 + rx)*8);
-            unsigned arr[4] = {raw.x, raw.y, raw.z, raw.w};
-            #pragma unroll
-            for (int e = 0; e < 8; ++e) {
-                ushort hv = (e & 1) ? (ushort)(arr[e>>1] >> 16) : (ushort)(arr[e>>1] & 0xffffu);
-                float f = fmaxf(fmaf(bf2f(hv), sc[cg*8 + e], sh[cg*8 + e]), 0.f);
-                acc = fmaf(f, wf[cg*8 + e][kk], acc);
-            }
-        }
-    }
-    satt[(size_t)b*P_ + pix] = 1.f / (1.f + expf(-acc));
+            if (x < 44) {
+                #pragma unroll
+                for (int og = 0; og < 2; ++og)
+                    #pragma unroll
+                    for (int mf = 0; mf < 2; ++mf)
+                        #pragma unroll
+                        for (int i = 0; i < 4; ++i) {
+                            int o = og*32 + mf*16 + lg*4 + i;
+                            out[(((size_t)b*64 + o)*44 + y)*44 + x] = fmaxf(acc[og][mf][nf][i] + bhf[o], 0.f);
+                        }
+            }
+        }
+    }
 }
 
 extern "C" void kernel_launch(void* const* d_in, const int* in_sizes, int n_in,
@@ -689,11 +705,12 @@
     float* out = (float*)d_out;
     float* ws  = (float*)d_ws;
 
-    float* satt  = ws;
-    float* catt  = satt + 30976;
-    float* dcor  = catt + 1024;
-    float* stats = dcor + 1024;
-    ushort* hcp    = (ushort*)(stats + 192);
+    float*    satt   = ws;
+    float*    catt   = satt + 30976;
+    float*    dcorp  = catt + 1024;
+    float*    stats  = dcorp + 4096;
+    unsigned* bar    = (unsigned*)(stats + 192);
+    ushort* hcp    = (ushort*)(bar + 8);
     ushort* wpck   = hcp    + 2355200;
     ushort* apck2  = wpck   + 147456;
     ushort* apck3  = apck2  + 9216;
@@ -705,17 +722,18 @@
     ushort* z3p    = z2p    + 1130496;
     ushort* xpck   = z3p    + 1130496;
 
-    k_setup<<<2936, 256, 0, stream>>>(w_hc, w_hf, w_s2, w_d1, w_s1, rgb, depth,
-                                      wpck, apck2, apck3, apck1, xpck, depthb, dcor, stats);
-
-    k_hcconv<<<dim3(11,2,16), 256, 0, stream>>>(xpck, wpck, b_hc, hcp);
-    k_Umfma<<<dim3(19,16), 256, 0, stream>>>(apck1, depthb, upck,
-                                             dcor, w_l1, bl1, w_l2, bl2, catt);
-
-    k_conv1_mfma<<<dim3(11,16), 256, 0, stream>>>(xpck, upck, bs1, z1p, stats);
-    k_conv2_mfma<<<dim3(10,16), 256, 0, stream>>>(z1p, apck2, bs2, g1, be1, stats, z2p, stats + 64);
-    k_dconv1_mfma<<<dim3(11,16), 256, 0, stream>>>(z2p, apck3, bd1, g2, be2, stats + 64, z3p, stats + 128);
-    k_dconv2<<<dim3(8,16), 256, 0, stream>>>(z3p, w_d2, bd2, g3, be3, stats + 128, satt);
-
-    k_final<<<dim3(11,2,16), 256, 0, stream>>>(hcp, satt, catt, wpck + 73728, b_hf, out);
+    k_setup<<<3320, 256, 0, stream>>>(w_hc, w_hf, w_s2, w_d1, w_s1, rgb, depth,
+                                      wpck, apck2, apck3, apck1, xpck, depthb,
+                                      dcorp, stats, bar);
+
+    k_front<<<480, 256, 0, stream>>>(xpck, wpck, b_hc, hcp,
+                                     apck1, depthb, upck,
+                                     dcorp, w_l1, bl1, w_l2, bl2, catt);
+
+    k_mid<<<dim3(11,16), 256, 0, stream>>>(xpck, upck, bs1,
+                                           apck2, bs2, g1, be1,
+                                           apck3, bd1, g2, be2,
+                                           w_d2, bd2, g3, be3,
+                                           hcp, catt, wpck + 73728, b_hf,
+                                           z1p, z2p, z3p, satt, stats, bar, out);
 }
```

New measurement: 163.2 us. 1.04x slower.
